# Kernel tuning notes

Hardware: AMD Instinct MI355X
Metric: run time of the kernel (lower is better)

Reference implementation:

```python
import jax, jax.numpy as jnp
import numpy as np

B, T, D = 256, 1024, 64          # batch, timesteps, num motor units (input_dim)
H, IC_DIM, F_DIM = 128, 100, 3   # hidden_dim, IC_dim, factors_dim


def setup_inputs() -> dict:
    key = jax.random.key(0)
    ks = jax.random.split(key, 16)
    s = 0.08  # ~1/sqrt(H) scale like torch default init
    f32 = jnp.float32
    return {
        "mu_batch": jax.random.normal(ks[0], (B, T, D), f32),
        # Encoder GRU (input D -> hidden H), PyTorch gate order [r, z, n]
        "We_ih": jax.random.normal(ks[1], (3 * H, D), f32) * s,
        "We_hh": jax.random.normal(ks[2], (3 * H, H), f32) * s,
        "be_ih": jax.random.normal(ks[3], (3 * H,), f32) * s,
        "be_hh": jax.random.normal(ks[4], (3 * H,), f32) * s,
        # IC layer H -> IC_DIM
        "W_ic": jax.random.normal(ks[5], (IC_DIM, H), f32) * s,
        "b_ic": jax.random.normal(ks[6], (IC_DIM,), f32) * s,
        # Generator GRU (input IC_DIM -> hidden H)
        "Wg_ih": jax.random.normal(ks[7], (3 * H, IC_DIM), f32) * s,
        "Wg_hh": jax.random.normal(ks[8], (3 * H, H), f32) * s,
        "bg_ih": jax.random.normal(ks[9], (3 * H,), f32) * s,
        "bg_hh": jax.random.normal(ks[10], (3 * H,), f32) * s,
        # GenToFactors H -> F_DIM
        "W_gf": jax.random.normal(ks[11], (F_DIM, H), f32) * s,
        "b_gf": jax.random.normal(ks[12], (F_DIM,), f32) * s,
        # FactorsToRates F_DIM -> D
        "W_fr": jax.random.normal(ks[13], (D, F_DIM), f32) * s,
        "b_fr": jax.random.normal(ks[14], (D,), f32) * s,
    }


def _gru_step(W_hh, b_hh):
    """PyTorch GRU cell: x_proj = W_ih @ x + b_ih precomputed, gate order r,z,n."""
    def step(h, x_proj):
        gh = h @ W_hh.T + b_hh
        xr, xz, xn = jnp.split(x_proj, 3, axis=-1)
        hr, hz, hn = jnp.split(gh, 3, axis=-1)
        r = jax.nn.sigmoid(xr + hr)
        z = jax.nn.sigmoid(xz + hz)
        n = jnp.tanh(xn + r * hn)
        h_new = (1.0 - z) * n + z * h
        return h_new, h_new
    return step


def reference(mu_batch, We_ih, We_hh, be_ih, be_hh, W_ic, b_ic,
              Wg_ih, Wg_hh, bg_ih, bg_hh, W_gf, b_gf, W_fr, b_fr):
    Bsz, Tlen, _ = mu_batch.shape
    Hdim = We_hh.shape[1]
    h0 = jnp.zeros((Bsz, Hdim), mu_batch.dtype)

    # ----- Encoder GRU: only final hidden state is used -----
    x_proj = jnp.einsum('btd,gd->btg', mu_batch, We_ih) + be_ih   # [B,T,3H]
    h_enc, _ = jax.lax.scan(_gru_step(We_hh, be_hh), h0,
                            jnp.swapaxes(x_proj, 0, 1))           # [B,H]

    # ----- IC layer -----
    IC = h_enc @ W_ic.T + b_ic                                    # [B,IC]

    # ----- Generator GRU: constant input IC fed for T steps, init hidden = h_enc -----
    ic_proj = IC @ Wg_ih.T + bg_ih                                # [B,3H], constant per step
    gstep = _gru_step(Wg_hh, bg_hh)
    def gen_step(h, _):
        return gstep(h, ic_proj)
    _, gen_out = jax.lax.scan(gen_step, h_enc, None, length=Tlen) # [T,B,H]
    gen_out = jnp.swapaxes(gen_out, 0, 1)                         # [B,T,H] == full_gen_out

    # ----- Readout -----
    factors = jnp.einsum('bth,fh->btf', gen_out, W_gf) + b_gf     # [B,T,F]
    rates = jnp.einsum('btf,df->btd', jnp.exp(factors), W_fr) + b_fr  # [B,T,D]
    return rates
```

## Files before the change

### kernel.cpp

```cpp
#include <hip/hip_runtime.h>
#include <hip/hip_bf16.h>

#define Bn 256
#define Tn 1024
#define Dn 64
#define Hn 128
#define G3 384
#define ICn 100
#define BT 16
#define NTH 512
#define LDH 136
#define LDX 72

typedef _Float16 f16;
typedef __attribute__((ext_vector_type(8))) _Float16 f16x8;
typedef __attribute__((ext_vector_type(4))) _Float16 f16x4;
typedef __attribute__((ext_vector_type(4))) float f32x4;

#define MFMA(a, b, c) __builtin_amdgcn_mfma_f32_16x16x32_f16((a), (b), (c), 0, 0, 0)

__device__ __forceinline__ float rcpa(float x) { return __builtin_amdgcn_rcpf(x); }
__device__ __forceinline__ float sigm(float x) { return rcpa(1.0f + __expf(-x)); }
__device__ __forceinline__ float tanha(float x) {
    float t = __expf(-2.0f * x);
    return fmaf(2.0f, rcpa(1.0f + t), -1.0f);
}

__device__ __forceinline__ f16x8 ldw(const float* W, int row, int ldk, int k0) {
    const float* p = W + (size_t)row * ldk + k0;
    f16x8 r;
#pragma unroll
    for (int j = 0; j < 8; ++j) r[j] = (f16)p[j];
    return r;
}

__global__ __launch_bounds__(NTH, 2)
void enc_kernel(const float* __restrict__ mu,
                const float* __restrict__ We_ih, const float* __restrict__ We_hh,
                const float* __restrict__ be_ih, const float* __restrict__ be_hh,
                float* __restrict__ h_enc)
{
    const int b0 = blockIdx.x * BT;
    const int tid = threadIdx.x;
    const int w = tid >> 6, l = tid & 63, c = l & 15, q = l >> 4;

    __shared__ f16 hbuf[2][BT * LDH];
    __shared__ f16 xstg[2][8][BT * LDX];

    const int gr = w * 16 + c, gz = Hn + w * 16 + c, gn = 2 * Hn + w * 16 + c;

    f16x8 whf[3][4], wxf[3][2];
#pragma unroll
    for (int kt = 0; kt < 4; ++kt) {
        whf[0][kt] = ldw(We_hh, gr, Hn, kt * 32 + q * 8);
        whf[1][kt] = ldw(We_hh, gz, Hn, kt * 32 + q * 8);
        whf[2][kt] = ldw(We_hh, gn, Hn, kt * 32 + q * 8);
    }
#pragma unroll
    for (int kt = 0; kt < 2; ++kt) {
        wxf[0][kt] = ldw(We_ih, gr, Dn, kt * 32 + q * 8);
        wxf[1][kt] = ldw(We_ih, gz, Dn, kt * 32 + q * 8);
        wxf[2][kt] = ldw(We_ih, gn, Dn, kt * 32 + q * 8);
    }
    const float brc = be_ih[gr] + be_hh[gr];
    const float bzc = be_ih[gz] + be_hh[gz];
    const float bxn = be_ih[gn];
    const float bhn = be_hh[gn];

    float hreg[4];
#pragma unroll
    for (int r4 = 0; r4 < 4; ++r4) hreg[r4] = 0.0f;
    for (int i = tid; i < BT * Hn; i += NTH) hbuf[0][(i >> 7) * LDH + (i & 127)] = (f16)0.0f;

    const int SIT = (BT * 8 * Dn) / (NTH * 4);
#pragma unroll
    for (int i = 0; i < SIT; ++i) {
        int f = (i * NTH + tid) * 4;
        int t_off = f >> 10, rem = f & 1023;
        int bb = rem >> 6, d = rem & 63;
        const float4 v = *reinterpret_cast<const float4*>(
            mu + ((size_t)(b0 + bb) * Tn + t_off) * Dn + d);
        f16x4 h4; h4[0] = (f16)v.x; h4[1] = (f16)v.y; h4[2] = (f16)v.z; h4[3] = (f16)v.w;
        *reinterpret_cast<f16x4*>(&xstg[0][t_off][bb * LDX + d]) = h4;
    }
    __syncthreads();

    float4 pre[SIT];
    for (int t = 0; t < Tn; ++t) {
        const int ch = t >> 3, s = t & 7, cur = t & 1, sb = ch & 1;
        if (s == 0 && ch + 1 < Tn / 8) {
#pragma unroll
            for (int i = 0; i < SIT; ++i) {
                int f = (i * NTH + tid) * 4;
                int t_off = f >> 10, rem = f & 1023;
                int bb = rem >> 6, d = rem & 63;
                pre[i] = *reinterpret_cast<const float4*>(
                    mu + ((size_t)(b0 + bb) * Tn + (ch + 1) * 8 + t_off) * Dn + d);
            }
        }
        f16x8 ah[4], ax[2];
#pragma unroll
        for (int kt = 0; kt < 4; ++kt)
            ah[kt] = *reinterpret_cast<const f16x8*>(&hbuf[cur][c * LDH + kt * 32 + q * 8]);
#pragma unroll
        for (int kt = 0; kt < 2; ++kt)
            ax[kt] = *reinterpret_cast<const f16x8*>(&xstg[sb][s][c * LDX + kt * 32 + q * 8]);

        f32x4 acc0 = (f32x4){0,0,0,0}, acc1 = (f32x4){0,0,0,0};
        f32x4 acc2 = (f32x4){0,0,0,0}, accx = (f32x4){0,0,0,0};
#pragma unroll
        for (int kt = 0; kt < 4; ++kt) {
            acc0 = MFMA(ah[kt], whf[0][kt], acc0);
            acc1 = MFMA(ah[kt], whf[1][kt], acc1);
            acc2 = MFMA(ah[kt], whf[2][kt], acc2);
        }
#pragma unroll
        for (int kt = 0; kt < 2; ++kt) {
            acc0 = MFMA(ax[kt], wxf[0][kt], acc0);
            acc1 = MFMA(ax[kt], wxf[1][kt], acc1);
            accx = MFMA(ax[kt], wxf[2][kt], accx);
        }
#pragma unroll
        for (int r4 = 0; r4 < 4; ++r4) {
            float rg = sigm(acc0[r4] + brc);
            float zg = sigm(acc1[r4] + bzc);
            float hn = acc2[r4] + bhn;
            float xn = accx[r4] + bxn;
            float ng = tanha(fmaf(rg, hn, xn));
            float hv = fmaf(zg, hreg[r4] - ng, ng);
            hreg[r4] = hv;
            hbuf[cur ^ 1][(q * 4 + r4) * LDH + w * 16 + c] = (f16)hv;
        }
        if (s == 7 && ch + 1 < Tn / 8) {
#pragma unroll
            for (int i = 0; i < SIT; ++i) {
                int f = (i * NTH + tid) * 4;
                int t_off = f >> 10, rem = f & 1023;
                int bb = rem >> 6, d = rem & 63;
                f16x4 h4;
                h4[0] = (f16)pre[i].x; h4[1] = (f16)pre[i].y;
                h4[2] = (f16)pre[i].z; h4[3] = (f16)pre[i].w;
                *reinterpret_cast<f16x4*>(&xstg[sb ^ 1][t_off][bb * LDX + d]) = h4;
            }
        }
        __syncthreads();
    }
#pragma unroll
    for (int r4 = 0; r4 < 4; ++r4)
        h_enc[(size_t)(b0 + q * 4 + r4) * Hn + w * 16 + c] = hreg[r4];
}

__global__ __launch_bounds__(NTH, 2)
void gen_kernel(const float* __restrict__ h_enc,
                const float* __restrict__ W_ic, const float* __restrict__ b_ic,
                const float* __restrict__ Wg_ih, const float* __restrict__ Wg_hh,
                const float* __restrict__ bg_ih, const float* __restrict__ bg_hh,
                const float* __restrict__ W_gf, const float* __restrict__ b_gf,
                const float* __restrict__ W_fr, const float* __restrict__ b_fr,
                float* __restrict__ out)
{
    const int b0 = blockIdx.x * BT;
    const int tid = threadIdx.x;
    const int w = tid >> 6, l = tid & 63, c = l & 15, q = l >> 4;

    __shared__ f16 hbuf[2][BT * LDH];
    __shared__ float hencs[BT][Hn];
    __shared__ float ics[BT][ICn];
    __shared__ float xpcs[BT][G3];
    __shared__ float fred[2][BT][4];

    for (int i = tid; i < BT * Hn; i += NTH)
        hencs[i >> 7][i & 127] = h_enc[(size_t)(b0 + (i >> 7)) * Hn + (i & 127)];
    __syncthreads();

    for (int i = tid; i < BT * ICn; i += NTH) {
        int bb = i / ICn, j = i - bb * ICn;
        float a = b_ic[j];
        const float* wr = W_ic + (size_t)j * Hn;
#pragma unroll 4
        for (int k = 0; k < Hn; ++k) a = fmaf(wr[k], hencs[bb][k], a);
        ics[bb][j] = a;
    }
    __syncthreads();

    for (int i = tid; i < BT * G3; i += NTH) {
        int g = i >> 4, bb = i & 15;
        float a = bg_ih[g];
        const float* wr = Wg_ih + (size_t)g * ICn;
#pragma unroll 4
        for (int k = 0; k < ICn; ++k) a = fmaf(wr[k], ics[bb][k], a);
        xpcs[bb][g] = a;
    }
    for (int i = tid; i < BT * Hn; i += NTH)
        hbuf[0][(i >> 7) * LDH + (i & 127)] = (f16)hencs[i >> 7][i & 127];

    const int gr = w * 16 + c, gz = Hn + w * 16 + c, gn = 2 * Hn + w * 16 + c;

    f16x8 whf[3][4];
#pragma unroll
    for (int kt = 0; kt < 4; ++kt) {
        whf[0][kt] = ldw(Wg_hh, gr, Hn, kt * 32 + q * 8);
        whf[1][kt] = ldw(Wg_hh, gz, Hn, kt * 32 + q * 8);
        whf[2][kt] = ldw(Wg_hh, gn, Hn, kt * 32 + q * 8);
    }
    f16x8 wgff[4];
    if (w == 0) {
#pragma unroll
        for (int kt = 0; kt < 4; ++kt) {
            if (c < 3) wgff[kt] = ldw(W_gf, c, Hn, kt * 32 + q * 8);
            else {
                f16x8 z;
#pragma unroll
                for (int j = 0; j < 8; ++j) z[j] = (f16)0.0f;
                wgff[kt] = z;
            }
        }
    }
    const float bgfc = (w == 0 && c < 3) ? b_gf[c] : 0.0f;
    const int d = l;
    const float wfr0 = W_fr[d * 3 + 0], wfr1 = W_fr[d * 3 + 1], wfr2 = W_fr[d * 3 + 2];
    const float bfrd = b_fr[d];

    float hreg[4];
#pragma unroll
    for (int r4 = 0; r4 < 4; ++r4) hreg[r4] = hencs[q * 4 + r4][w * 16 + c];

    __syncthreads();

    const float bgr = bg_hh[gr], bgz = bg_hh[gz], bhn = bg_hh[gn];
    float xrc[4], xzc[4], xnc[4];
#pragma unroll
    for (int r4 = 0; r4 < 4; ++r4) {
        int bb = q * 4 + r4;
        xrc[r4] = xpcs[bb][gr] + bgr;
        xzc[r4] = xpcs[bb][gz] + bgz;
        xnc[r4] = xpcs[bb][gn];
    }

    for (int t = 0; t < Tn; ++t) {
        const int cur = t & 1;
        f16x8 ah[4];
#pragma unroll
        for (int kt = 0; kt < 4; ++kt)
            ah[kt] = *reinterpret_cast<const f16x8*>(&hbuf[cur][c * LDH + kt * 32 + q * 8]);

        f32x4 acc0 = (f32x4){0,0,0,0}, acc1 = (f32x4){0,0,0,0}, acc2 = (f32x4){0,0,0,0};
#pragma unroll
        for (int kt = 0; kt < 4; ++kt) {
            acc0 = MFMA(ah[kt], whf[0][kt], acc0);
            acc1 = MFMA(ah[kt], whf[1][kt], acc1);
            acc2 = MFMA(ah[kt], whf[2][kt], acc2);
        }
        f32x4 facc = (f32x4){0, 0, 0, 0};
        if (w == 0) {
#pragma unroll
            for (int kt = 0; kt < 4; ++kt) facc = MFMA(ah[kt], wgff[kt], facc);
        }
#pragma unroll
        for (int r4 = 0; r4 < 4; ++r4) {
            float rg = sigm(acc0[r4] + xrc[r4]);
            float zg = sigm(acc1[r4] + xzc[r4]);
            float hn = acc2[r4] + bhn;
            float ng = tanha(fmaf(rg, hn, xnc[r4]));
            float hv = fmaf(zg, hreg[r4] - ng, ng);
            hreg[r4] = hv;
            hbuf[cur ^ 1][(q * 4 + r4) * LDH + w * 16 + c] = (f16)hv;
        }
        if (w == 0 && c < 3) {
#pragma unroll
            for (int r4 = 0; r4 < 4; ++r4)
                fred[cur][q * 4 + r4][c] = __expf(facc[r4] + bgfc);
        }
        __syncthreads();
        if (t >= 1) {
            const int tout = t - 1;
#pragma unroll
            for (int rb = 0; rb < 2; ++rb) {
                int bb = w + rb * 8;
                float e0 = fred[cur][bb][0], e1 = fred[cur][bb][1], e2 = fred[cur][bb][2];
                float rate = bfrd + e0 * wfr0 + e1 * wfr1 + e2 * wfr2;
                out[((size_t)(b0 + bb) * Tn + tout) * Dn + d] = rate;
            }
        }
    }
    if (w == 0) {
        f16x8 ah[4];
#pragma unroll
        for (int kt = 0; kt < 4; ++kt)
            ah[kt] = *reinterpret_cast<const f16x8*>(&hbuf[0][c * LDH + kt * 32 + q * 8]);
        f32x4 facc = (f32x4){0, 0, 0, 0};
#pragma unroll
        for (int kt = 0; kt < 4; ++kt) facc = MFMA(ah[kt], wgff[kt], facc);
        if (c < 3) {
#pragma unroll
            for (int r4 = 0; r4 < 4; ++r4)
                fred[0][q * 4 + r4][c] = __expf(facc[r4] + bgfc);
        }
    }
    __syncthreads();
    {
#pragma unroll
        for (int rb = 0; rb < 2; ++rb) {
            int bb = w + rb * 8;
            float e0 = fred[0][bb][0], e1 = fred[0][bb][1], e2 = fred[0][bb][2];
            float rate = bfrd + e0 * wfr0 + e1 * wfr1 + e2 * wfr2;
            out[((size_t)(b0 + bb) * Tn + (Tn - 1)) * Dn + d] = rate;
        }
    }
}

extern "C" void kernel_launch(void* const* d_in, const int* in_sizes, int n_in,
                              void* d_out, int out_size, void* d_ws, size_t ws_size,
                              hipStream_t stream) {
    const float* mu    = (const float*)d_in[0];
    const float* We_ih = (const float*)d_in[1];
    const float* We_hh = (const float*)d_in[2];
    const float* be_ih = (const float*)d_in[3];
    const float* be_hh = (const float*)d_in[4];
    const float* W_ic  = (const float*)d_in[5];
    const float* b_ic  = (const float*)d_in[6];
    const float* Wg_ih = (const float*)d_in[7];
    const float* Wg_hh = (const float*)d_in[8];
    const float* bg_ih = (const float*)d_in[9];
    const float* bg_hh = (const float*)d_in[10];
    const float* W_gf  = (const float*)d_in[11];
    const float* b_gf  = (const float*)d_in[12];
    const float* W_fr  = (const float*)d_in[13];
    const float* b_fr  = (const float*)d_in[14];

    float* h_enc = (float*)d_ws;
    float* out = (float*)d_out;

    enc_kernel<<<dim3(Bn / BT), dim3(NTH), 0, stream>>>(mu, We_ih, We_hh, be_ih, be_hh, h_enc);
    gen_kernel<<<dim3(Bn / BT), dim3(NTH), 0, stream>>>(h_enc, W_ic, b_ic, Wg_ih, Wg_hh,
                                                        bg_ih, bg_hh, W_gf, b_gf, W_fr, b_fr, out);
}
```

Before: 1.613 ms.

## Prefetch encoder inputs into registers, rotate readout wave, use Newton reciprocal

The encoder drops the shared-memory staging of mu. Each lane instead prefetches its next-timestep input directly from global memory into registers, double buffered, and converts it to f16 in place. The time loops in both kernels are unrolled by two with fixed buffer pointers. The generator's factor-readout MFMA and exp now rotate across waves instead of always landing on wave 0, and fred is read with float4 loads. The hardware rcp is replaced by a bit-trick initial guess refined with two Newton iterations, which adds ALU work and possibly changes precision. Per-step global loads in the encoder may add latency on the serial critical path.

```diff
diff --git a/kernel.cpp b/kernel.cpp
--- a/kernel.cpp
+++ b/kernel.cpp
@@ -10,20 +10,26 @@
 #define BT 16
 #define NTH 512
 #define LDH 136
-#define LDX 72
 
 typedef _Float16 f16;
 typedef __attribute__((ext_vector_type(8))) _Float16 f16x8;
-typedef __attribute__((ext_vector_type(4))) _Float16 f16x4;
 typedef __attribute__((ext_vector_type(4))) float f32x4;
 
 #define MFMA(a, b, c) __builtin_amdgcn_mfma_f32_16x16x32_f16((a), (b), (c), 0, 0, 0)
 
-__device__ __forceinline__ float rcpa(float x) { return __builtin_amdgcn_rcpf(x); }
-__device__ __forceinline__ float sigm(float x) { return rcpa(1.0f + __expf(-x)); }
+__device__ __forceinline__ float nrcp(float d) {
+    float y = __uint_as_float(0x7ef311c3u - __float_as_uint(d));
+    y = y * (2.0f - d * y);
+    y = y * (2.0f - d * y);
+    return y;
+}
+__device__ __forceinline__ float sigm(float x) {
+    float t = fminf(__expf(-x), 3e37f);
+    return nrcp(1.0f + t);
+}
 __device__ __forceinline__ float tanha(float x) {
-    float t = __expf(-2.0f * x);
-    return fmaf(2.0f, rcpa(1.0f + t), -1.0f);
+    float t = fminf(__expf(-2.0f * x), 3e37f);
+    return fmaf(2.0f, nrcp(1.0f + t), -1.0f);
 }
 
 __device__ __forceinline__ f16x8 ldw(const float* W, int row, int ldk, int k0) {
@@ -45,7 +51,6 @@
     const int w = tid >> 6, l = tid & 63, c = l & 15, q = l >> 4;
 
     __shared__ f16 hbuf[2][BT * LDH];
-    __shared__ f16 xstg[2][8][BT * LDX];
 
     const int gr = w * 16 + c, gz = Hn + w * 16 + c, gn = 2 * Hn + w * 16 + c;
 
@@ -72,39 +77,36 @@
     for (int r4 = 0; r4 < 4; ++r4) hreg[r4] = 0.0f;
     for (int i = tid; i < BT * Hn; i += NTH) hbuf[0][(i >> 7) * LDH + (i & 127)] = (f16)0.0f;
 
-    const int SIT = (BT * 8 * Dn) / (NTH * 4);
-#pragma unroll
-    for (int i = 0; i < SIT; ++i) {
-        int f = (i * NTH + tid) * 4;
-        int t_off = f >> 10, rem = f & 1023;
-        int bb = rem >> 6, d = rem & 63;
-        const float4 v = *reinterpret_cast<const float4*>(
-            mu + ((size_t)(b0 + bb) * Tn + t_off) * Dn + d);
-        f16x4 h4; h4[0] = (f16)v.x; h4[1] = (f16)v.y; h4[2] = (f16)v.z; h4[3] = (f16)v.w;
-        *reinterpret_cast<f16x4*>(&xstg[0][t_off][bb * LDX + d]) = h4;
-    }
-    __syncthreads();
-
-    float4 pre[SIT];
-    for (int t = 0; t < Tn; ++t) {
-        const int ch = t >> 3, s = t & 7, cur = t & 1, sb = ch & 1;
-        if (s == 0 && ch + 1 < Tn / 8) {
-#pragma unroll
-            for (int i = 0; i < SIT; ++i) {
-                int f = (i * NTH + tid) * 4;
-                int t_off = f >> 10, rem = f & 1023;
-                int bb = rem >> 6, d = rem & 63;
-                pre[i] = *reinterpret_cast<const float4*>(
-                    mu + ((size_t)(b0 + bb) * Tn + (ch + 1) * 8 + t_off) * Dn + d);
-            }
-        }
-        f16x8 ah[4], ax[2];
+    const float* xp_base = mu + ((size_t)(b0 + c) * Tn) * Dn + q * 8;
+
+    float4 xbA[4], xbB[4];
+    xbA[0] = *reinterpret_cast<const float4*>(xp_base + 0);
+    xbA[1] = *reinterpret_cast<const float4*>(xp_base + 4);
+    xbA[2] = *reinterpret_cast<const float4*>(xp_base + 32);
+    xbA[3] = *reinterpret_cast<const float4*>(xp_base + 36);
+    __syncthreads();
+
+    auto step = [&](int t, float4* xcur, float4* xnxt, const f16* hb_r, f16* hb_w) {
+        if (t + 1 < Tn) {
+            const float* p = xp_base + (size_t)(t + 1) * Dn;
+            xnxt[0] = *reinterpret_cast<const float4*>(p + 0);
+            xnxt[1] = *reinterpret_cast<const float4*>(p + 4);
+            xnxt[2] = *reinterpret_cast<const float4*>(p + 32);
+            xnxt[3] = *reinterpret_cast<const float4*>(p + 36);
+        }
+        f16x8 ax[2];
+#pragma unroll
+        for (int kt = 0; kt < 2; ++kt) {
+            const float4 v0 = xcur[2 * kt], v1 = xcur[2 * kt + 1];
+            ax[kt][0] = (f16)v0.x; ax[kt][1] = (f16)v0.y;
+            ax[kt][2] = (f16)v0.z; ax[kt][3] = (f16)v0.w;
+            ax[kt][4] = (f16)v1.x; ax[kt][5] = (f16)v1.y;
+            ax[kt][6] = (f16)v1.z; ax[kt][7] = (f16)v1.w;
+        }
+        f16x8 ah[4];
 #pragma unroll
         for (int kt = 0; kt < 4; ++kt)
-            ah[kt] = *reinterpret_cast<const f16x8*>(&hbuf[cur][c * LDH + kt * 32 + q * 8]);
-#pragma unroll
-        for (int kt = 0; kt < 2; ++kt)
-            ax[kt] = *reinterpret_cast<const f16x8*>(&xstg[sb][s][c * LDX + kt * 32 + q * 8]);
+            ah[kt] = *reinterpret_cast<const f16x8*>(&hb_r[c * LDH + kt * 32 + q * 8]);
 
         f32x4 acc0 = (f32x4){0,0,0,0}, acc1 = (f32x4){0,0,0,0};
         f32x4 acc2 = (f32x4){0,0,0,0}, accx = (f32x4){0,0,0,0};
@@ -129,21 +131,14 @@
             float ng = tanha(fmaf(rg, hn, xn));
             float hv = fmaf(zg, hreg[r4] - ng, ng);
             hreg[r4] = hv;
-            hbuf[cur ^ 1][(q * 4 + r4) * LDH + w * 16 + c] = (f16)hv;
-        }
-        if (s == 7 && ch + 1 < Tn / 8) {
-#pragma unroll
-            for (int i = 0; i < SIT; ++i) {
-                int f = (i * NTH + tid) * 4;
-                int t_off = f >> 10, rem = f & 1023;
-                int bb = rem >> 6, d = rem & 63;
-                f16x4 h4;
-                h4[0] = (f16)pre[i].x; h4[1] = (f16)pre[i].y;
-                h4[2] = (f16)pre[i].z; h4[3] = (f16)pre[i].w;
-                *reinterpret_cast<f16x4*>(&xstg[sb ^ 1][t_off][bb * LDX + d]) = h4;
-            }
+            hb_w[(q * 4 + r4) * LDH + w * 16 + c] = (f16)hv;
         }
         __syncthreads();
+    };
+
+    for (int tt = 0; tt < Tn; tt += 2) {
+        step(tt,     xbA, xbB, hbuf[0], hbuf[1]);
+        step(tt + 1, xbB, xbA, hbuf[1], hbuf[0]);
     }
 #pragma unroll
     for (int r4 = 0; r4 < 4; ++r4)
@@ -204,22 +199,22 @@
         whf[2][kt] = ldw(Wg_hh, gn, Hn, kt * 32 + q * 8);
     }
     f16x8 wgff[4];
-    if (w == 0) {
-#pragma unroll
-        for (int kt = 0; kt < 4; ++kt) {
-            if (c < 3) wgff[kt] = ldw(W_gf, c, Hn, kt * 32 + q * 8);
-            else {
-                f16x8 z;
-#pragma unroll
-                for (int j = 0; j < 8; ++j) z[j] = (f16)0.0f;
-                wgff[kt] = z;
-            }
-        }
-    }
-    const float bgfc = (w == 0 && c < 3) ? b_gf[c] : 0.0f;
+#pragma unroll
+    for (int kt = 0; kt < 4; ++kt) {
+        if (c < 3) wgff[kt] = ldw(W_gf, c, Hn, kt * 32 + q * 8);
+        else {
+            f16x8 z;
+#pragma unroll
+            for (int j = 0; j < 8; ++j) z[j] = (f16)0.0f;
+            wgff[kt] = z;
+        }
+    }
+    const float bgfc = (c < 3) ? b_gf[c] : 0.0f;
     const int d = l;
     const float wfr0 = W_fr[d * 3 + 0], wfr1 = W_fr[d * 3 + 1], wfr2 = W_fr[d * 3 + 2];
     const float bfrd = b_fr[d];
+    float* op0 = out + ((size_t)(b0 + w) * Tn) * Dn + d;
+    float* op1 = out + ((size_t)(b0 + w + 8) * Tn) * Dn + d;
 
     float hreg[4];
 #pragma unroll
@@ -237,12 +232,12 @@
         xnc[r4] = xpcs[bb][gn];
     }
 
-    for (int t = 0; t < Tn; ++t) {
+    auto step = [&](int t, const f16* hb_r, f16* hb_w) {
         const int cur = t & 1;
         f16x8 ah[4];
 #pragma unroll
         for (int kt = 0; kt < 4; ++kt)
-            ah[kt] = *reinterpret_cast<const f16x8*>(&hbuf[cur][c * LDH + kt * 32 + q * 8]);
+            ah[kt] = *reinterpret_cast<const f16x8*>(&hb_r[c * LDH + kt * 32 + q * 8]);
 
         f32x4 acc0 = (f32x4){0,0,0,0}, acc1 = (f32x4){0,0,0,0}, acc2 = (f32x4){0,0,0,0};
 #pragma unroll
@@ -251,10 +246,15 @@
             acc1 = MFMA(ah[kt], whf[1][kt], acc1);
             acc2 = MFMA(ah[kt], whf[2][kt], acc2);
         }
-        f32x4 facc = (f32x4){0, 0, 0, 0};
-        if (w == 0) {
+        if (w == (t & 7)) {
+            f32x4 facc = (f32x4){0, 0, 0, 0};
 #pragma unroll
             for (int kt = 0; kt < 4; ++kt) facc = MFMA(ah[kt], wgff[kt], facc);
+            if (c < 3) {
+#pragma unroll
+                for (int r4 = 0; r4 < 4; ++r4)
+                    fred[cur][q * 4 + r4][c] = __expf(facc[r4] + bgfc);
+            }
         }
 #pragma unroll
         for (int r4 = 0; r4 < 4; ++r4) {
@@ -264,24 +264,21 @@
             float ng = tanha(fmaf(rg, hn, xnc[r4]));
             float hv = fmaf(zg, hreg[r4] - ng, ng);
             hreg[r4] = hv;
-            hbuf[cur ^ 1][(q * 4 + r4) * LDH + w * 16 + c] = (f16)hv;
-        }
-        if (w == 0 && c < 3) {
-#pragma unroll
-            for (int r4 = 0; r4 < 4; ++r4)
-                fred[cur][q * 4 + r4][c] = __expf(facc[r4] + bgfc);
+            hb_w[(q * 4 + r4) * LDH + w * 16 + c] = (f16)hv;
         }
         __syncthreads();
         if (t >= 1) {
-            const int tout = t - 1;
-#pragma unroll
-            for (int rb = 0; rb < 2; ++rb) {
-                int bb = w + rb * 8;
-                float e0 = fred[cur][bb][0], e1 = fred[cur][bb][1], e2 = fred[cur][bb][2];
-                float rate = bfrd + e0 * wfr0 + e1 * wfr1 + e2 * wfr2;
-                out[((size_t)(b0 + bb) * Tn + tout) * Dn + d] = rate;
-            }
-        }
+            const size_t ofs = (size_t)(t - 1) * Dn;
+            const float4 f0 = *reinterpret_cast<const float4*>(&fred[cur][w][0]);
+            op0[ofs] = bfrd + f0.x * wfr0 + f0.y * wfr1 + f0.z * wfr2;
+            const float4 f1 = *reinterpret_cast<const float4*>(&fred[cur][w + 8][0]);
+            op1[ofs] = bfrd + f1.x * wfr0 + f1.y * wfr1 + f1.z * wfr2;
+        }
+    };
+
+    for (int tt = 0; tt < Tn; tt += 2) {
+        step(tt,     hbuf[0], hbuf[1]);
+        step(tt + 1, hbuf[1], hbuf[0]);
     }
     if (w == 0) {
         f16x8 ah[4];
@@ -299,13 +296,11 @@
     }
     __syncthreads();
     {
-#pragma unroll
-        for (int rb = 0; rb < 2; ++rb) {
-            int bb = w + rb * 8;
-            float e0 = fred[0][bb][0], e1 = fred[0][bb][1], e2 = fred[0][bb][2];
-            float rate = bfrd + e0 * wfr0 + e1 * wfr1 + e2 * wfr2;
-            out[((size_t)(b0 + bb) * Tn + (Tn - 1)) * Dn + d] = rate;
-        }
+        const size_t ofs = (size_t)(Tn - 1) * Dn;
+        const float4 f0 = *reinterpret_cast<const float4*>(&fred[0][w][0]);
+        op0[ofs] = bfrd + f0.x * wfr0 + f0.y * wfr1 + f0.z * wfr2;
+        const float4 f1 = *reinterpret_cast<const float4*>(&fred[0][w + 8][0]);
+        op1[ofs] = bfrd + f1.x * wfr0 + f1.y * wfr1 + f1.z * wfr2;
     }
 }
 
```

Result: slower. 2.243 ms (+39.1%).
